# Performance work log

Hardware: AMD Instinct MI355X
Metric: run time of the kernel (lower is better)

The kernel has to match this reference:

```python
import jax, jax.numpy as jnp
import numpy as np

D_K = 64
SCALE = 1.0 / (D_K ** 0.5)
NEG_INF = float('-inf')


def setup_inputs() -> dict:
    key = jax.random.key(0)
    kq, kk, kv = jax.random.split(key, 3)
    B, H, S, D = 2, 16, 2048, D_K
    Q = jax.random.normal(kq, (B, H, S, D), dtype=jnp.float32)
    K = jax.random.normal(kk, (B, H, S, D), dtype=jnp.float32)
    V = jax.random.normal(kv, (B, H, S, D), dtype=jnp.float32)
    # causal mask: True = attend, False = masked (matches masked_fill(mask == False, -inf))
    mask = jnp.tril(jnp.ones((S, S), dtype=jnp.bool_))
    return {"Q": Q, "K": K, "V": V, "mask": mask}


def reference(Q, K, V, mask):
    # scores: [B, H, q, k]
    scores = jnp.einsum('bhqd,bhkd->bhqk', Q, K) * SCALE
    scores = jnp.where(mask, scores, NEG_INF)
    # hand-rolled stable softmax, same math as the torch module
    x_exp = jnp.exp(scores - jnp.max(scores, axis=-1, keepdims=True))
    attn = x_exp / jnp.sum(x_exp, axis=-1, keepdims=True)
    out = jnp.einsum('bhqk,bhkv->bhqv', attn, V)
    return out
```

## Files before the change

kernel.cpp:

```cpp
#include <hip/hip_runtime.h>
#include <hip/hip_bf16.h>

#define S_LEN   2048
#define D_DIM   64
#define BK      64

typedef __attribute__((ext_vector_type(8))) short  short8;
typedef __attribute__((ext_vector_type(4))) float  floatx4;

#define KLD   72
#define VTLD  72
#define PLD   72
#define OLD   65

#define VTOFF 9216
#define POFF  18432
#define SMEM_BYTES 27648

__device__ __forceinline__ short f2bf(float x) {
  union { __hip_bfloat16 h; short s; } u;
  u.h = __float2bfloat16(x);
  return u.s;
}
__device__ __forceinline__ unsigned pk2(float lo, float hi) {
  union { __hip_bfloat16 h; unsigned short s; } a, b;
  a.h = __float2bfloat16(lo);
  b.h = __float2bfloat16(hi);
  return (unsigned)a.s | ((unsigned)b.s << 16);
}

__global__ __launch_bounds__(256, 2)
void fa_fwd(const float* __restrict__ Qg, const float* __restrict__ Kg,
            const float* __restrict__ Vg, float* __restrict__ Og)
{
  __shared__ char smem[SMEM_BYTES];
  short* Klds  = (short*)smem;
  short* Vtlds = (short*)(smem + VTOFF);

  const int tid  = threadIdx.x;
  const int wv   = tid >> 6;
  const int lane = tid & 63;
  const int col  = lane & 15;
  const int quad = lane >> 4;
  short* Plds = (short*)(smem + POFF) + wv * (16 * PLD);
  float* Olds = (float*)smem + wv * (16 * OLD);

  const int qblk = 31 - (blockIdx.x >> 5);
  const int bh   = blockIdx.x & 31;

  const float qscale = 0.18033688011112042f;
  const float* Kb = Kg + (size_t)bh * S_LEN * D_DIM;
  const float* Vb = Vg + (size_t)bh * S_LEN * D_DIM;
  const float* Qb = Qg + (size_t)bh * S_LEN * D_DIM;
  float*       Ob = Og + (size_t)bh * S_LEN * D_DIM;

  const int krow = tid >> 2;
  const int kcb  = (tid & 3) * 16;
  const int kp2  = tid & 31;
  const int dbs  = (tid >> 5) * 8;

  float4 kr[4], vr[4];

  const int q0  = qblk * 64;
  const int nit = qblk + 1;
  const int qw  = q0 + wv * 16;

  short8 qf[2];
#pragma unroll
  for (int h = 0; h < 2; ++h) {
    const float* qp = Qb + (size_t)(qw + col) * D_DIM + h * 32 + quad * 8;
    float4 a = *(const float4*)qp;
    float4 b = *(const float4*)(qp + 4);
    short8 f;
    f[0]=f2bf(a.x*qscale); f[1]=f2bf(a.y*qscale); f[2]=f2bf(a.z*qscale); f[3]=f2bf(a.w*qscale);
    f[4]=f2bf(b.x*qscale); f[5]=f2bf(b.y*qscale); f[6]=f2bf(b.z*qscale); f[7]=f2bf(b.w*qscale);
    qf[h] = f;
  }

  floatx4 o[4];
#pragma unroll
  for (int dt = 0; dt < 4; ++dt) o[dt] = (floatx4){0.f,0.f,0.f,0.f};
  float m_run = -3.0e38f, l_run = 0.f;

  {
    const float* p = Kb + (size_t)krow * D_DIM + kcb;
    kr[0] = *(const float4*)p;       kr[1] = *(const float4*)(p + 4);
    kr[2] = *(const float4*)(p + 8); kr[3] = *(const float4*)(p + 12);
    const float* pv = Vb + (size_t)(2 * kp2) * D_DIM + dbs;
    vr[0] = *(const float4*)pv;        vr[1] = *(const float4*)(pv + 4);
    vr[2] = *(const float4*)(pv + 64); vr[3] = *(const float4*)(pv + 68);
  }

  for (int it = 0; it < nit; ++it) {
    __syncthreads();

    {
      const float* f = (const float*)kr;
      short8 f0, f1;
      f0[0]=f2bf(f[0]);  f0[1]=f2bf(f[1]);  f0[2]=f2bf(f[2]);  f0[3]=f2bf(f[3]);
      f0[4]=f2bf(f[4]);  f0[5]=f2bf(f[5]);  f0[6]=f2bf(f[6]);  f0[7]=f2bf(f[7]);
      f1[0]=f2bf(f[8]);  f1[1]=f2bf(f[9]);  f1[2]=f2bf(f[10]); f1[3]=f2bf(f[11]);
      f1[4]=f2bf(f[12]); f1[5]=f2bf(f[13]); f1[6]=f2bf(f[14]); f1[7]=f2bf(f[15]);
      *(short8*)&Klds[krow * KLD + kcb]     = f0;
      *(short8*)&Klds[krow * KLD + kcb + 8] = f1;
      const float* g = (const float*)vr;
#pragma unroll
      for (int i = 0; i < 8; ++i)
        *(unsigned*)&Vtlds[(dbs + i) * VTLD + 2 * kp2] = pk2(g[i], g[8 + i]);
    }
    __syncthreads();

    if (it + 1 < nit) {
      const int kb2 = (it + 1) * BK;
      const float* p = Kb + (size_t)(kb2 + krow) * D_DIM + kcb;
      kr[0] = *(const float4*)p;       kr[1] = *(const float4*)(p + 4);
      kr[2] = *(const float4*)(p + 8); kr[3] = *(const float4*)(p + 12);
      const float* pv = Vb + (size_t)(kb2 + 2 * kp2) * D_DIM + dbs;
      vr[0] = *(const float4*)pv;        vr[1] = *(const float4*)(pv + 4);
      vr[2] = *(const float4*)(pv + 64); vr[3] = *(const float4*)(pv + 68);
    }

    short8 kf[4][2];
#pragma unroll
    for (int kt = 0; kt < 4; ++kt)
#pragma unroll
      for (int h = 0; h < 2; ++h)
        kf[kt][h] = *(short8*)&Klds[(kt * 16 + col) * KLD + h * 32 + quad * 8];

    floatx4 st[4];
#pragma unroll
    for (int kt = 0; kt < 4; ++kt) {
      floatx4 c = (floatx4){0.f,0.f,0.f,0.f};
      c = __builtin_amdgcn_mfma_f32_16x16x32_bf16(kf[kt][0], qf[0], c, 0, 0, 0);
      c = __builtin_amdgcn_mfma_f32_16x16x32_bf16(kf[kt][1], qf[1], c, 0, 0, 0);
      st[kt] = c;
    }

    if (it == nit - 1) {
      const int qg = qw + col;
      const int kb = it * BK;
#pragma unroll
      for (int kt = 0; kt < 4; ++kt)
#pragma unroll
        for (int r = 0; r < 4; ++r)
          if (kb + kt * 16 + quad * 4 + r > qg) st[kt][r] = -3.0e38f;
    }

    float mx = st[0][0];
#pragma unroll
    for (int kt = 0; kt < 4; ++kt)
#pragma unroll
      for (int r = 0; r < 4; ++r) mx = fmaxf(mx, st[kt][r]);
    mx = fmaxf(mx, __shfl_xor(mx, 16));
    mx = fmaxf(mx, __shfl_xor(mx, 32));
    const float mnew  = fmaxf(m_run, mx);
    const float alpha = __builtin_amdgcn_exp2f(m_run - mnew);
    m_run = mnew;
    float sum = 0.f;
#pragma unroll
    for (int kt = 0; kt < 4; ++kt)
#pragma unroll
      for (int r = 0; r < 4; ++r) {
        const float p = __builtin_amdgcn_exp2f(st[kt][r] - mnew);
        st[kt][r] = p;
        sum += p;
      }
    sum += __shfl_xor(sum, 16);
    sum += __shfl_xor(sum, 32);
    l_run = l_run * alpha + sum;
#pragma unroll
    for (int dt = 0; dt < 4; ++dt)
#pragma unroll
      for (int r = 0; r < 4; ++r) o[dt][r] *= alpha;

#pragma unroll
    for (int kt = 0; kt < 4; ++kt) {
      *(unsigned*)&Plds[col * PLD + kt * 16 + quad * 4]     = pk2(st[kt][0], st[kt][1]);
      *(unsigned*)&Plds[col * PLD + kt * 16 + quad * 4 + 2] = pk2(st[kt][2], st[kt][3]);
    }
    short8 pf0 = *(short8*)&Plds[col * PLD + quad * 8];
    short8 pf1 = *(short8*)&Plds[col * PLD + 32 + quad * 8];

#pragma unroll
    for (int dt = 0; dt < 4; ++dt) {
      short8 vf0 = *(short8*)&Vtlds[(dt * 16 + col) * VTLD + quad * 8];
      short8 vf1 = *(short8*)&Vtlds[(dt * 16 + col) * VTLD + 32 + quad * 8];
      o[dt] = __builtin_amdgcn_mfma_f32_16x16x32_bf16(vf0, pf0, o[dt], 0, 0, 0);
      o[dt] = __builtin_amdgcn_mfma_f32_16x16x32_bf16(vf1, pf1, o[dt], 0, 0, 0);
    }
  }

  __syncthreads();
  const float inv = 1.0f / l_run;
#pragma unroll
  for (int dt = 0; dt < 4; ++dt)
#pragma unroll
    for (int r = 0; r < 4; ++r)
      Olds[col * OLD + dt * 16 + quad * 4 + r] = o[dt][r] * inv;
#pragma unroll
  for (int it2 = 0; it2 < 4; ++it2) {
    const int ql = it2 * 4 + quad;
    float4 w;
    w.x = Olds[ql * OLD + col * 4 + 0];
    w.y = Olds[ql * OLD + col * 4 + 1];
    w.z = Olds[ql * OLD + col * 4 + 2];
    w.w = Olds[ql * OLD + col * 4 + 3];
    *(float4*)(Ob + (size_t)(qw + ql) * D_DIM + col * 4) = w;
  }
}

extern "C" void kernel_launch(void* const* d_in, const int* in_sizes, int n_in,
                              void* d_out, int out_size, void* d_ws, size_t ws_size,
                              hipStream_t stream) {
  const float* Q = (const float*)d_in[0];
  const float* K = (const float*)d_in[1];
  const float* V = (const float*)d_in[2];
  float* O = (float*)d_out;
  dim3 grid(32 * 32);
  dim3 block(256);
  hipLaunchKernelGGL(fa_fwd, grid, block, 0, stream, Q, K, V, O);
}
```

Measured before the change: 145.0 us.

## Double-buffer K/V tiles in LDS to drop one barrier per iteration

Splits the K and transposed-V LDS staging into two ping-pong buffers. The first tile is converted and stored before the loop. Each later tile is converted to bf16 and written into the alternate buffer after the current tile's MFMAs, so each iteration needs only one __syncthreads instead of two. This cuts barrier stalls and lets the LDS stores overlap other waves' compute, at the cost of LDS growing from about 27 KB to 46 KB per block, which could limit occupancy.

```diff
diff --git a/kernel.cpp b/kernel.cpp
--- a/kernel.cpp
+++ b/kernel.cpp
@@ -13,9 +13,12 @@
 #define PLD   72
 #define OLD   65
 
-#define VTOFF 9216
-#define POFF  18432
-#define SMEM_BYTES 27648
+#define K0OFF 0
+#define K1OFF 9216
+#define V0OFF 18432
+#define V1OFF 27648
+#define POFF  36864
+#define SMEM_BYTES 46080
 
 __device__ __forceinline__ short f2bf(float x) {
   union { __hip_bfloat16 h; short s; } u;
@@ -34,8 +37,6 @@
             const float* __restrict__ Vg, float* __restrict__ Og)
 {
   __shared__ char smem[SMEM_BYTES];
-  short* Klds  = (short*)smem;
-  short* Vtlds = (short*)(smem + VTOFF);
 
   const int tid  = threadIdx.x;
   const int wv   = tid >> 6;
@@ -58,8 +59,6 @@
   const int kcb  = (tid & 3) * 16;
   const int kp2  = tid & 31;
   const int dbs  = (tid >> 5) * 8;
-
-  float4 kr[4], vr[4];
 
   const int q0  = qblk * 64;
   const int nit = qblk + 1;
@@ -82,6 +81,8 @@
   for (int dt = 0; dt < 4; ++dt) o[dt] = (floatx4){0.f,0.f,0.f,0.f};
   float m_run = -3.0e38f, l_run = 0.f;
 
+  float4 kr[4], vr[4];
+
   {
     const float* p = Kb + (size_t)krow * D_DIM + kcb;
     kr[0] = *(const float4*)p;       kr[1] = *(const float4*)(p + 4);
@@ -89,28 +90,33 @@
     const float* pv = Vb + (size_t)(2 * kp2) * D_DIM + dbs;
     vr[0] = *(const float4*)pv;        vr[1] = *(const float4*)(pv + 4);
     vr[2] = *(const float4*)(pv + 64); vr[3] = *(const float4*)(pv + 68);
-  }
+
+    short* K0 = (short*)(smem + K0OFF);
+    short* V0 = (short*)(smem + V0OFF);
+    const float* f = (const float*)kr;
+    short8 f0, f1;
+    f0[0]=f2bf(f[0]);  f0[1]=f2bf(f[1]);  f0[2]=f2bf(f[2]);  f0[3]=f2bf(f[3]);
+    f0[4]=f2bf(f[4]);  f0[5]=f2bf(f[5]);  f0[6]=f2bf(f[6]);  f0[7]=f2bf(f[7]);
+    f1[0]=f2bf(f[8]);  f1[1]=f2bf(f[9]);  f1[2]=f2bf(f[10]); f1[3]=f2bf(f[11]);
+    f1[4]=f2bf(f[12]); f1[5]=f2bf(f[13]); f1[6]=f2bf(f[14]); f1[7]=f2bf(f[15]);
+    *(short8*)&K0[krow * KLD + kcb]     = f0;
+    *(short8*)&K0[krow * KLD + kcb + 8] = f1;
+    const float* g = (const float*)vr;
+#pragma unroll
+    for (int i = 0; i < 8; ++i)
+      *(unsigned*)&V0[(dbs + i) * VTLD + 2 * kp2] = pk2(g[i], g[8 + i]);
+  }
+  __syncthreads();
 
   for (int it = 0; it < nit; ++it) {
-    __syncthreads();
-
-    {
-      const float* f = (const float*)kr;
-      short8 f0, f1;
-      f0[0]=f2bf(f[0]);  f0[1]=f2bf(f[1]);  f0[2]=f2bf(f[2]);  f0[3]=f2bf(f[3]);
-      f0[4]=f2bf(f[4]);  f0[5]=f2bf(f[5]);  f0[6]=f2bf(f[6]);  f0[7]=f2bf(f[7]);
-      f1[0]=f2bf(f[8]);  f1[1]=f2bf(f[9]);  f1[2]=f2bf(f[10]); f1[3]=f2bf(f[11]);
-      f1[4]=f2bf(f[12]); f1[5]=f2bf(f[13]); f1[6]=f2bf(f[14]); f1[7]=f2bf(f[15]);
-      *(short8*)&Klds[krow * KLD + kcb]     = f0;
-      *(short8*)&Klds[krow * KLD + kcb + 8] = f1;
-      const float* g = (const float*)vr;
-#pragma unroll
-      for (int i = 0; i < 8; ++i)
-        *(unsigned*)&Vtlds[(dbs + i) * VTLD + 2 * kp2] = pk2(g[i], g[8 + i]);
-    }
-    __syncthreads();
-
-    if (it + 1 < nit) {
+    const int cur = it & 1;
+    short* Kc = (short*)(smem + (cur ? K1OFF : K0OFF));
+    short* Vc = (short*)(smem + (cur ? V1OFF : V0OFF));
+    short* Kn = (short*)(smem + (cur ? K0OFF : K1OFF));
+    short* Vn = (short*)(smem + (cur ? V0OFF : V1OFF));
+
+    const bool have_next = (it + 1 < nit);
+    if (have_next) {
       const int kb2 = (it + 1) * BK;
       const float* p = Kb + (size_t)(kb2 + krow) * D_DIM + kcb;
       kr[0] = *(const float4*)p;       kr[1] = *(const float4*)(p + 4);
@@ -125,7 +131,7 @@
     for (int kt = 0; kt < 4; ++kt)
 #pragma unroll
       for (int h = 0; h < 2; ++h)
-        kf[kt][h] = *(short8*)&Klds[(kt * 16 + col) * KLD + h * 32 + quad * 8];
+        kf[kt][h] = *(short8*)&Kc[(kt * 16 + col) * KLD + h * 32 + quad * 8];
 
     floatx4 st[4];
 #pragma unroll
@@ -183,14 +189,29 @@
 
 #pragma unroll
     for (int dt = 0; dt < 4; ++dt) {
-      short8 vf0 = *(short8*)&Vtlds[(dt * 16 + col) * VTLD + quad * 8];
-      short8 vf1 = *(short8*)&Vtlds[(dt * 16 + col) * VTLD + 32 + quad * 8];
+      short8 vf0 = *(short8*)&Vc[(dt * 16 + col) * VTLD + quad * 8];
+      short8 vf1 = *(short8*)&Vc[(dt * 16 + col) * VTLD + 32 + quad * 8];
       o[dt] = __builtin_amdgcn_mfma_f32_16x16x32_bf16(vf0, pf0, o[dt], 0, 0, 0);
       o[dt] = __builtin_amdgcn_mfma_f32_16x16x32_bf16(vf1, pf1, o[dt], 0, 0, 0);
     }
-  }
-
-  __syncthreads();
+
+    if (have_next) {
+      const float* f = (const float*)kr;
+      short8 f0, f1;
+      f0[0]=f2bf(f[0]);  f0[1]=f2bf(f[1]);  f0[2]=f2bf(f[2]);  f0[3]=f2bf(f[3]);
+      f0[4]=f2bf(f[4]);  f0[5]=f2bf(f[5]);  f0[6]=f2bf(f[6]);  f0[7]=f2bf(f[7]);
+      f1[0]=f2bf(f[8]);  f1[1]=f2bf(f[9]);  f1[2]=f2bf(f[10]); f1[3]=f2bf(f[11]);
+      f1[4]=f2bf(f[12]); f1[5]=f2bf(f[13]); f1[6]=f2bf(f[14]); f1[7]=f2bf(f[15]);
+      *(short8*)&Kn[krow * KLD + kcb]     = f0;
+      *(short8*)&Kn[krow * KLD + kcb + 8] = f1;
+      const float* g = (const float*)vr;
+#pragma unroll
+      for (int i = 0; i < 8; ++i)
+        *(unsigned*)&Vn[(dbs + i) * VTLD + 2 * kp2] = pk2(g[i], g[8 + i]);
+    }
+    __syncthreads();
+  }
+
   const float inv = 1.0f / l_run;
 #pragma unroll
   for (int dt = 0; dt < 4; ++dt)
```

Result: no change. 145.7 us (+0.5%).

## Double the K/V tile to 128 keys per iteration and pack bf16 conversions

Applied to the files above, without the earlier changes.

Raises the key-block size from 64 to 128, which halves the number of loop iterations and the barrier/softmax-rescale overhead per query block. The K/V staging, transposed V layout and P buffer are resized, and the per-thread global-load mapping is changed to match. It also swaps scalar bf16 conversions for paired float2-to-bf16x2 conversions. The trade-offs are doubled LDS use (about 52KB) and more registers, which may hurt the two-blocks-per-CU occupancy target. Causal diagonal blocks now also compute up to 64 extra masked keys.

```diff
diff --git a/kernel.cpp b/kernel.cpp
--- a/kernel.cpp
+++ b/kernel.cpp
@@ -3,30 +3,30 @@
 
 #define S_LEN   2048
 #define D_DIM   64
-#define BK      64
+#define BK      128
 
 typedef __attribute__((ext_vector_type(8))) short  short8;
 typedef __attribute__((ext_vector_type(4))) float  floatx4;
 
 #define KLD   72
-#define VTLD  72
-#define PLD   72
+#define VTLD  136
+#define PLD   136
 #define OLD   65
 
-#define VTOFF 9216
-#define POFF  18432
-#define SMEM_BYTES 27648
-
-__device__ __forceinline__ short f2bf(float x) {
-  union { __hip_bfloat16 h; short s; } u;
-  u.h = __float2bfloat16(x);
-  return u.s;
-}
+#define VOFF  18432
+#define POFF  35840
+#define SMEM_BYTES 53248
+
 __device__ __forceinline__ unsigned pk2(float lo, float hi) {
-  union { __hip_bfloat16 h; unsigned short s; } a, b;
-  a.h = __float2bfloat16(lo);
-  b.h = __float2bfloat16(hi);
-  return (unsigned)a.s | ((unsigned)b.s << 16);
+  __hip_bfloat162 h = __float22bfloat162_rn(float2{lo, hi});
+  union { __hip_bfloat162 v; unsigned u; } c; c.v = h;
+  return c.u;
+}
+__device__ __forceinline__ short8 pk8(const float* f) {
+  union { short8 s; unsigned u[4]; } r;
+  r.u[0] = pk2(f[0], f[1]); r.u[1] = pk2(f[2], f[3]);
+  r.u[2] = pk2(f[4], f[5]); r.u[3] = pk2(f[6], f[7]);
+  return r.s;
 }
 
 __global__ __launch_bounds__(256, 2)
@@ -35,7 +35,7 @@
 {
   __shared__ char smem[SMEM_BYTES];
   short* Klds  = (short*)smem;
-  short* Vtlds = (short*)(smem + VTOFF);
+  short* Vtlds = (short*)(smem + VOFF);
 
   const int tid  = threadIdx.x;
   const int wv   = tid >> 6;
@@ -54,15 +54,13 @@
   const float* Qb = Qg + (size_t)bh * S_LEN * D_DIM;
   float*       Ob = Og + (size_t)bh * S_LEN * D_DIM;
 
-  const int krow = tid >> 2;
-  const int kcb  = (tid & 3) * 16;
-  const int kp2  = tid & 31;
-  const int dbs  = (tid >> 5) * 8;
-
-  float4 kr[4], vr[4];
+  const int krow = tid >> 1;
+  const int kcb  = (tid & 1) * 32;
+  const int kp2  = tid & 63;
+  const int dgrp = (tid >> 6) * 16;
 
   const int q0  = qblk * 64;
-  const int nit = qblk + 1;
+  const int nit = (q0 + 64 + BK - 1) / BK;
   const int qw  = q0 + wv * 16;
 
   short8 qf[2];
@@ -71,10 +69,9 @@
     const float* qp = Qb + (size_t)(qw + col) * D_DIM + h * 32 + quad * 8;
     float4 a = *(const float4*)qp;
     float4 b = *(const float4*)(qp + 4);
-    short8 f;
-    f[0]=f2bf(a.x*qscale); f[1]=f2bf(a.y*qscale); f[2]=f2bf(a.z*qscale); f[3]=f2bf(a.w*qscale);
-    f[4]=f2bf(b.x*qscale); f[5]=f2bf(b.y*qscale); f[6]=f2bf(b.z*qscale); f[7]=f2bf(b.w*qscale);
-    qf[h] = f;
+    float t[8] = {a.x*qscale, a.y*qscale, a.z*qscale, a.w*qscale,
+                  b.x*qscale, b.y*qscale, b.z*qscale, b.w*qscale};
+    qf[h] = pk8(t);
   }
 
   floatx4 o[4];
@@ -82,13 +79,18 @@
   for (int dt = 0; dt < 4; ++dt) o[dt] = (floatx4){0.f,0.f,0.f,0.f};
   float m_run = -3.0e38f, l_run = 0.f;
 
+  float4 kr[8], vr[8];
+
   {
     const float* p = Kb + (size_t)krow * D_DIM + kcb;
-    kr[0] = *(const float4*)p;       kr[1] = *(const float4*)(p + 4);
-    kr[2] = *(const float4*)(p + 8); kr[3] = *(const float4*)(p + 12);
-    const float* pv = Vb + (size_t)(2 * kp2) * D_DIM + dbs;
-    vr[0] = *(const float4*)pv;        vr[1] = *(const float4*)(pv + 4);
-    vr[2] = *(const float4*)(pv + 64); vr[3] = *(const float4*)(pv + 68);
+#pragma unroll
+    for (int j = 0; j < 8; ++j) kr[j] = *(const float4*)(p + 4*j);
+    const float* pv = Vb + (size_t)(2 * kp2) * D_DIM + dgrp;
+#pragma unroll
+    for (int j = 0; j < 4; ++j) {
+      vr[j]     = *(const float4*)(pv + 4*j);
+      vr[4 + j] = *(const float4*)(pv + D_DIM + 4*j);
+    }
   }
 
   for (int it = 0; it < nit; ++it) {
@@ -96,43 +98,38 @@
 
     {
       const float* f = (const float*)kr;
-      short8 f0, f1;
-      f0[0]=f2bf(f[0]);  f0[1]=f2bf(f[1]);  f0[2]=f2bf(f[2]);  f0[3]=f2bf(f[3]);
-      f0[4]=f2bf(f[4]);  f0[5]=f2bf(f[5]);  f0[6]=f2bf(f[6]);  f0[7]=f2bf(f[7]);
-      f1[0]=f2bf(f[8]);  f1[1]=f2bf(f[9]);  f1[2]=f2bf(f[10]); f1[3]=f2bf(f[11]);
-      f1[4]=f2bf(f[12]); f1[5]=f2bf(f[13]); f1[6]=f2bf(f[14]); f1[7]=f2bf(f[15]);
-      *(short8*)&Klds[krow * KLD + kcb]     = f0;
-      *(short8*)&Klds[krow * KLD + kcb + 8] = f1;
-      const float* g = (const float*)vr;
-#pragma unroll
-      for (int i = 0; i < 8; ++i)
-        *(unsigned*)&Vtlds[(dbs + i) * VTLD + 2 * kp2] = pk2(g[i], g[8 + i]);
+#pragma unroll
+      for (int j = 0; j < 4; ++j)
+        *(short8*)&Klds[krow * KLD + kcb + 8*j] = pk8(f + 8*j);
+      const float* glo = (const float*)vr;
+      const float* ghi = (const float*)(vr + 4);
+#pragma unroll
+      for (int i = 0; i < 16; ++i)
+        *(unsigned*)&Vtlds[(dgrp + i) * VTLD + 2 * kp2] = pk2(glo[i], ghi[i]);
     }
     __syncthreads();
 
     if (it + 1 < nit) {
       const int kb2 = (it + 1) * BK;
       const float* p = Kb + (size_t)(kb2 + krow) * D_DIM + kcb;
-      kr[0] = *(const float4*)p;       kr[1] = *(const float4*)(p + 4);
-      kr[2] = *(const float4*)(p + 8); kr[3] = *(const float4*)(p + 12);
-      const float* pv = Vb + (size_t)(kb2 + 2 * kp2) * D_DIM + dbs;
-      vr[0] = *(const float4*)pv;        vr[1] = *(const float4*)(pv + 4);
-      vr[2] = *(const float4*)(pv + 64); vr[3] = *(const float4*)(pv + 68);
-    }
-
-    short8 kf[4][2];
-#pragma unroll
-    for (int kt = 0; kt < 4; ++kt)
-#pragma unroll
-      for (int h = 0; h < 2; ++h)
-        kf[kt][h] = *(short8*)&Klds[(kt * 16 + col) * KLD + h * 32 + quad * 8];
-
-    floatx4 st[4];
-#pragma unroll
-    for (int kt = 0; kt < 4; ++kt) {
+#pragma unroll
+      for (int j = 0; j < 8; ++j) kr[j] = *(const float4*)(p + 4*j);
+      const float* pv = Vb + (size_t)(kb2 + 2 * kp2) * D_DIM + dgrp;
+#pragma unroll
+      for (int j = 0; j < 4; ++j) {
+        vr[j]     = *(const float4*)(pv + 4*j);
+        vr[4 + j] = *(const float4*)(pv + D_DIM + 4*j);
+      }
+    }
+
+    floatx4 st[8];
+#pragma unroll
+    for (int kt = 0; kt < 8; ++kt) {
+      short8 kf0 = *(short8*)&Klds[(kt * 16 + col) * KLD + quad * 8];
+      short8 kf1 = *(short8*)&Klds[(kt * 16 + col) * KLD + 32 + quad * 8];
       floatx4 c = (floatx4){0.f,0.f,0.f,0.f};
-      c = __builtin_amdgcn_mfma_f32_16x16x32_bf16(kf[kt][0], qf[0], c, 0, 0, 0);
-      c = __builtin_amdgcn_mfma_f32_16x16x32_bf16(kf[kt][1], qf[1], c, 0, 0, 0);
+      c = __builtin_amdgcn_mfma_f32_16x16x32_bf16(kf0, qf[0], c, 0, 0, 0);
+      c = __builtin_amdgcn_mfma_f32_16x16x32_bf16(kf1, qf[1], c, 0, 0, 0);
       st[kt] = c;
     }
 
@@ -140,7 +137,7 @@
       const int qg = qw + col;
       const int kb = it * BK;
 #pragma unroll
-      for (int kt = 0; kt < 4; ++kt)
+      for (int kt = 0; kt < 8; ++kt)
 #pragma unroll
         for (int r = 0; r < 4; ++r)
           if (kb + kt * 16 + quad * 4 + r > qg) st[kt][r] = -3.0e38f;
@@ -148,7 +145,7 @@
 
     float mx = st[0][0];
 #pragma unroll
-    for (int kt = 0; kt < 4; ++kt)
+    for (int kt = 0; kt < 8; ++kt)
 #pragma unroll
       for (int r = 0; r < 4; ++r) mx = fmaxf(mx, st[kt][r]);
     mx = fmaxf(mx, __shfl_xor(mx, 16));
@@ -158,7 +155,7 @@
     m_run = mnew;
     float sum = 0.f;
 #pragma unroll
-    for (int kt = 0; kt < 4; ++kt)
+    for (int kt = 0; kt < 8; ++kt)
 #pragma unroll
       for (int r = 0; r < 4; ++r) {
         const float p = __builtin_amdgcn_exp2f(st[kt][r] - mnew);
@@ -174,19 +171,19 @@
       for (int r = 0; r < 4; ++r) o[dt][r] *= alpha;
 
 #pragma unroll
-    for (int kt = 0; kt < 4; ++kt) {
-      *(unsigned*)&Plds[col * PLD + kt * 16 + quad * 4]     = pk2(st[kt][0], st[kt][1]);
-      *(unsigned*)&Plds[col * PLD + kt * 16 + quad * 4 + 2] = pk2(st[kt][2], st[kt][3]);
-    }
-    short8 pf0 = *(short8*)&Plds[col * PLD + quad * 8];
-    short8 pf1 = *(short8*)&Plds[col * PLD + 32 + quad * 8];
-
-#pragma unroll
-    for (int dt = 0; dt < 4; ++dt) {
-      short8 vf0 = *(short8*)&Vtlds[(dt * 16 + col) * VTLD + quad * 8];
-      short8 vf1 = *(short8*)&Vtlds[(dt * 16 + col) * VTLD + 32 + quad * 8];
-      o[dt] = __builtin_amdgcn_mfma_f32_16x16x32_bf16(vf0, pf0, o[dt], 0, 0, 0);
-      o[dt] = __builtin_amdgcn_mfma_f32_16x16x32_bf16(vf1, pf1, o[dt], 0, 0, 0);
+    for (int kt = 0; kt < 8; ++kt) {
+      uint2 w; w.x = pk2(st[kt][0], st[kt][1]); w.y = pk2(st[kt][2], st[kt][3]);
+      *(uint2*)&Plds[col * PLD + kt * 16 + quad * 4] = w;
+    }
+
+#pragma unroll
+    for (int g = 0; g < 4; ++g) {
+      short8 pf = *(short8*)&Plds[col * PLD + g * 32 + quad * 8];
+#pragma unroll
+      for (int dt = 0; dt < 4; ++dt) {
+        short8 vf = *(short8*)&Vtlds[(dt * 16 + col) * VTLD + g * 32 + quad * 8];
+        o[dt] = __builtin_amdgcn_mfma_f32_16x16x32_bf16(vf, pf, o[dt], 0, 0, 0);
+      }
     }
   }
 
```

New measurement: 166.6 us. +14.9%, slower.

## Precompute bf16 K and transposed bf16 V in a prep kernel

Applied to the files above, without the earlier changes.

Adds a separate prep kernel that converts K to bf16 and writes V transposed in bf16 into workspace. The attention kernel then streams half-width data and copies it straight into LDS, with no per-tile conversion or scattered transpose stores. This removes redundant fp32 loads and conversions that were repeated by every query block sharing a head. The cost is an extra launch and an extra write and read of the converted tensors through global memory. Conversion helpers also switch to packed bf16x2 intrinsics.

```diff
diff --git a/kernel.cpp b/kernel.cpp
--- a/kernel.cpp
+++ b/kernel.cpp
@@ -4,6 +4,7 @@
 #define S_LEN   2048
 #define D_DIM   64
 #define BK      64
+#define NBH     32
 
 typedef __attribute__((ext_vector_type(8))) short  short8;
 typedef __attribute__((ext_vector_type(4))) float  floatx4;
@@ -13,29 +14,74 @@
 #define PLD   72
 #define OLD   65
 
-#define VTOFF 9216
+#define VOFF  9216
 #define POFF  18432
 #define SMEM_BYTES 27648
 
-__device__ __forceinline__ short f2bf(float x) {
-  union { __hip_bfloat16 h; short s; } u;
-  u.h = __float2bfloat16(x);
-  return u.s;
-}
 __device__ __forceinline__ unsigned pk2(float lo, float hi) {
-  union { __hip_bfloat16 h; unsigned short s; } a, b;
-  a.h = __float2bfloat16(lo);
-  b.h = __float2bfloat16(hi);
-  return (unsigned)a.s | ((unsigned)b.s << 16);
+  __hip_bfloat162 h = __float22bfloat162_rn(float2{lo, hi});
+  union { __hip_bfloat162 v; unsigned u; } c; c.v = h;
+  return c.u;
+}
+__device__ __forceinline__ short8 pk8(const float* f) {
+  union { short8 s; unsigned u[4]; } r;
+  r.u[0] = pk2(f[0], f[1]); r.u[1] = pk2(f[2], f[3]);
+  r.u[2] = pk2(f[4], f[5]); r.u[3] = pk2(f[6], f[7]);
+  return r.s;
 }
 
 __global__ __launch_bounds__(256, 2)
-void fa_fwd(const float* __restrict__ Qg, const float* __restrict__ Kg,
-            const float* __restrict__ Vg, float* __restrict__ Og)
+void prep(const float* __restrict__ K, const float* __restrict__ V,
+          unsigned short* __restrict__ Kbf, unsigned short* __restrict__ Vt)
+{
+  __shared__ unsigned short vt[64 * KLD];
+  const int tid = threadIdx.x;
+  const int bh  = blockIdx.x >> 5;
+  const int k0  = (blockIdx.x & 31) * 64;
+
+  {
+    const int k   = k0 + (tid >> 2);
+    const int seg = (tid & 3) * 16;
+    const float* p = K + ((size_t)(bh * S_LEN + k)) * D_DIM + seg;
+    union { float4 v[4]; float f[16]; } u;
+    u.v[0] = *(const float4*)p;      u.v[1] = *(const float4*)(p + 4);
+    u.v[2] = *(const float4*)(p + 8); u.v[3] = *(const float4*)(p + 12);
+    unsigned short* dst = Kbf + ((size_t)(bh * S_LEN + k)) * D_DIM + seg;
+    *(short8*)dst       = pk8(u.f);
+    *(short8*)(dst + 8) = pk8(u.f + 8);
+  }
+  {
+    const int kp2 = tid & 31;
+    const int dg  = (tid >> 5) * 8;
+    const float* p = V + ((size_t)(bh * S_LEN + k0 + 2 * kp2)) * D_DIM + dg;
+    union { float4 v[2]; float f[8]; } x, y;
+    x.v[0] = *(const float4*)p;            x.v[1] = *(const float4*)(p + 4);
+    y.v[0] = *(const float4*)(p + D_DIM);  y.v[1] = *(const float4*)(p + D_DIM + 4);
+#pragma unroll
+    for (int i = 0; i < 8; ++i)
+      *(unsigned*)&vt[(dg + i) * KLD + 2 * kp2] = pk2(x.f[i], y.f[i]);
+  }
+  __syncthreads();
+  {
+    const int d   = tid >> 2;
+    const int seg = (tid & 3) * 16;
+    short8 a = *(short8*)&vt[d * KLD + seg];
+    short8 b = *(short8*)&vt[d * KLD + seg + 8];
+    unsigned short* dst = Vt + ((size_t)(bh * D_DIM + d)) * S_LEN + k0 + seg;
+    *(short8*)dst       = a;
+    *(short8*)(dst + 8) = b;
+  }
+}
+
+__global__ __launch_bounds__(256, 2)
+void fa_fwd(const float* __restrict__ Qg,
+            const unsigned short* __restrict__ Kbf,
+            const unsigned short* __restrict__ Vt,
+            float* __restrict__ Og)
 {
   __shared__ char smem[SMEM_BYTES];
   short* Klds  = (short*)smem;
-  short* Vtlds = (short*)(smem + VTOFF);
+  short* Vtlds = (short*)(smem + VOFF);
 
   const int tid  = threadIdx.x;
   const int wv   = tid >> 6;
@@ -49,17 +95,13 @@
   const int bh   = blockIdx.x & 31;
 
   const float qscale = 0.18033688011112042f;
-  const float* Kb = Kg + (size_t)bh * S_LEN * D_DIM;
-  const float* Vb = Vg + (size_t)bh * S_LEN * D_DIM;
-  const float* Qb = Qg + (size_t)bh * S_LEN * D_DIM;
-  float*       Ob = Og + (size_t)bh * S_LEN * D_DIM;
-
-  const int krow = tid >> 2;
-  const int kcb  = (tid & 3) * 16;
-  const int kp2  = tid & 31;
-  const int dbs  = (tid >> 5) * 8;
-
-  float4 kr[4], vr[4];
+  const float*          Qb  = Qg  + (size_t)bh * S_LEN * D_DIM;
+  const unsigned short* Kb  = Kbf + (size_t)bh * S_LEN * D_DIM;
+  const unsigned short* Vtb = Vt  + (size_t)bh * D_DIM * S_LEN;
+  float*                Ob  = Og  + (size_t)bh * S_LEN * D_DIM;
+
+  const int srow = tid >> 2;
+  const int sseg = (tid & 3) * 16;
 
   const int q0  = qblk * 64;
   const int nit = qblk + 1;
@@ -69,12 +111,12 @@
 #pragma unroll
   for (int h = 0; h < 2; ++h) {
     const float* qp = Qb + (size_t)(qw + col) * D_DIM + h * 32 + quad * 8;
-    float4 a = *(const float4*)qp;
-    float4 b = *(const float4*)(qp + 4);
-    short8 f;
-    f[0]=f2bf(a.x*qscale); f[1]=f2bf(a.y*qscale); f[2]=f2bf(a.z*qscale); f[3]=f2bf(a.w*qscale);
-    f[4]=f2bf(b.x*qscale); f[5]=f2bf(b.y*qscale); f[6]=f2bf(b.z*qscale); f[7]=f2bf(b.w*qscale);
-    qf[h] = f;
+    union { float4 v[2]; float f[8]; } u;
+    u.v[0] = *(const float4*)qp; u.v[1] = *(const float4*)(qp + 4);
+    float t[8];
+#pragma unroll
+    for (int j = 0; j < 8; ++j) t[j] = u.f[j] * qscale;
+    qf[h] = pk8(t);
   }
 
   floatx4 o[4];
@@ -82,42 +124,30 @@
   for (int dt = 0; dt < 4; ++dt) o[dt] = (floatx4){0.f,0.f,0.f,0.f};
   float m_run = -3.0e38f, l_run = 0.f;
 
-  {
-    const float* p = Kb + (size_t)krow * D_DIM + kcb;
-    kr[0] = *(const float4*)p;       kr[1] = *(const float4*)(p + 4);
-    kr[2] = *(const float4*)(p + 8); kr[3] = *(const float4*)(p + 12);
-    const float* pv = Vb + (size_t)(2 * kp2) * D_DIM + dbs;
-    vr[0] = *(const float4*)pv;        vr[1] = *(const float4*)(pv + 4);
-    vr[2] = *(const float4*)(pv + 64); vr[3] = *(const float4*)(pv + 68);
+  short8 kpre[2], vpre[2];
+
+  {
+    const unsigned short* kp = Kb  + (size_t)srow * D_DIM + sseg;
+    kpre[0] = *(const short8*)kp;  kpre[1] = *(const short8*)(kp + 8);
+    const unsigned short* vp = Vtb + (size_t)srow * S_LEN + sseg;
+    vpre[0] = *(const short8*)vp;  vpre[1] = *(const short8*)(vp + 8);
   }
 
   for (int it = 0; it < nit; ++it) {
     __syncthreads();
 
-    {
-      const float* f = (const float*)kr;
-      short8 f0, f1;
-      f0[0]=f2bf(f[0]);  f0[1]=f2bf(f[1]);  f0[2]=f2bf(f[2]);  f0[3]=f2bf(f[3]);
-      f0[4]=f2bf(f[4]);  f0[5]=f2bf(f[5]);  f0[6]=f2bf(f[6]);  f0[7]=f2bf(f[7]);
-      f1[0]=f2bf(f[8]);  f1[1]=f2bf(f[9]);  f1[2]=f2bf(f[10]); f1[3]=f2bf(f[11]);
-      f1[4]=f2bf(f[12]); f1[5]=f2bf(f[13]); f1[6]=f2bf(f[14]); f1[7]=f2bf(f[15]);
-      *(short8*)&Klds[krow * KLD + kcb]     = f0;
-      *(short8*)&Klds[krow * KLD + kcb + 8] = f1;
-      const float* g = (const float*)vr;
-#pragma unroll
-      for (int i = 0; i < 8; ++i)
-        *(unsigned*)&Vtlds[(dbs + i) * VTLD + 2 * kp2] = pk2(g[i], g[8 + i]);
-    }
+    *(short8*)&Klds [srow * KLD  + sseg]     = kpre[0];
+    *(short8*)&Klds [srow * KLD  + sseg + 8] = kpre[1];
+    *(short8*)&Vtlds[srow * VTLD + sseg]     = vpre[0];
+    *(short8*)&Vtlds[srow * VTLD + sseg + 8] = vpre[1];
     __syncthreads();
 
     if (it + 1 < nit) {
       const int kb2 = (it + 1) * BK;
-      const float* p = Kb + (size_t)(kb2 + krow) * D_DIM + kcb;
-      kr[0] = *(const float4*)p;       kr[1] = *(const float4*)(p + 4);
-      kr[2] = *(const float4*)(p + 8); kr[3] = *(const float4*)(p + 12);
-      const float* pv = Vb + (size_t)(kb2 + 2 * kp2) * D_DIM + dbs;
-      vr[0] = *(const float4*)pv;        vr[1] = *(const float4*)(pv + 4);
-      vr[2] = *(const float4*)(pv + 64); vr[3] = *(const float4*)(pv + 68);
+      const unsigned short* kp = Kb  + (size_t)(kb2 + srow) * D_DIM + sseg;
+      kpre[0] = *(const short8*)kp;  kpre[1] = *(const short8*)(kp + 8);
+      const unsigned short* vp = Vtb + (size_t)srow * S_LEN + kb2 + sseg;
+      vpre[0] = *(const short8*)vp;  vpre[1] = *(const short8*)(vp + 8);
     }
 
     short8 kf[4][2];
@@ -175,8 +205,8 @@
 
 #pragma unroll
     for (int kt = 0; kt < 4; ++kt) {
-      *(unsigned*)&Plds[col * PLD + kt * 16 + quad * 4]     = pk2(st[kt][0], st[kt][1]);
-      *(unsigned*)&Plds[col * PLD + kt * 16 + quad * 4 + 2] = pk2(st[kt][2], st[kt][3]);
+      uint2 w; w.x = pk2(st[kt][0], st[kt][1]); w.y = pk2(st[kt][2], st[kt][3]);
+      *(uint2*)&Plds[col * PLD + kt * 16 + quad * 4] = w;
     }
     short8 pf0 = *(short8*)&Plds[col * PLD + quad * 8];
     short8 pf1 = *(short8*)&Plds[col * PLD + 32 + quad * 8];
@@ -216,7 +246,9 @@
   const float* K = (const float*)d_in[1];
   const float* V = (const float*)d_in[2];
   float* O = (float*)d_out;
-  dim3 grid(32 * 32);
-  dim3 block(256);
-  hipLaunchKernelGGL(fa_fwd, grid, block, 0, stream, Q, K, V, O);
-}
+  unsigned short* Kbf = (unsigned short*)d_ws;
+  unsigned short* Vt  = Kbf + (size_t)NBH * S_LEN * D_DIM;
+
+  hipLaunchKernelGGL(prep,  dim3(NBH * (S_LEN / 64)), dim3(256), 0, stream, K, V, Kbf, Vt);
+  hipLaunchKernelGGL(fa_fwd, dim3(32 * NBH), dim3(256), 0, stream, Q, Kbf, Vt, O);
+}
```

Result: no change. 145.8 us (+0.6%).
